# Optimization experiments

Measured on AMD Instinct MI355X. Metric: run time of the kernel, lower is better.

## Reference

```python
import jax, jax.numpy as jnp
import numpy as np

B, IN, OUT, T = 64, 1024, 512, 512
V_TH = 1.0
TAU = 16.0


def alpha_kernel(t, tau):
    # SRM alpha kernel: (t/tau)*exp(1 - t/tau) for t > 0, else 0.
    # Mask BEFORE exp to avoid overflow for large negative t.
    ts = jnp.where(t > 0, t, tau)
    v = (ts / tau) * jnp.exp(1.0 - ts / tau)
    return jnp.where(t > 0, v, 0.0)


def setup_inputs() -> dict:
    key = jax.random.key(0)
    k1, k2 = jax.random.split(key)
    # input spike times in [0, T/2)
    in_spike = jax.random.uniform(k1, (B, IN), dtype=jnp.float32) * (T / 2)
    weight = jax.random.normal(k2, (OUT, IN), dtype=jnp.float32) / np.float32(np.sqrt(IN))
    return {"in_spike": in_spike, "weight": weight}


def reference(in_spike, weight):
    t_seq = jnp.arange(T, dtype=jnp.float32)                  # [T]
    time_sequence = t_seq[None, None, :] - in_spike[:, :, None]  # [B, in, T]
    v_input = alpha_kernel(time_sequence, TAU)                 # [B, in, T]
    # fc applied along the `in` axis at every time step
    membrane_voltage = jnp.einsum('bit,oi->bot', v_input, weight)  # [B, out, T]
    # first time index where voltage crosses threshold; T if never.
    mask = membrane_voltage >= V_TH                            # [B, out, T]
    spiked = mask.any(axis=-1)
    first_t = jnp.argmax(mask, axis=-1)                        # first True index
    out_spike = jnp.where(spiked, first_t, T).astype(jnp.float32)  # [B, out]
    return out_spike
```

## Files before the change

kernel.cpp:

```cpp
#include <hip/hip_runtime.h>
#include <math.h>

#define BATCH   64
#define INS     1024
#define OUTS    512
#define TSTEPS  512
#define TAUF    16.0f

#define TT 64
#define NTRANS ((INS / TT) * (OUTS / TT))

__global__ __launch_bounds__(256) void pre_kernel(
        const float* __restrict__ w, float* __restrict__ wT,
        const float* __restrict__ in_spike, float4* __restrict__ spk) {
    __shared__ float tile[TT][TT + 1];
    __shared__ int hist[257];
    __shared__ int cursor[257];
    __shared__ int scanbuf[256];

    if (blockIdx.x < NTRANS) {
        const int i0 = (blockIdx.x & (INS / TT - 1)) * TT;
        const int o0 = (blockIdx.x / (INS / TT)) * TT;
        const int c  = threadIdx.x & 63;
        const int r  = threadIdx.x >> 6;
#pragma unroll
        for (int rr = r; rr < TT; rr += 4)
            tile[rr][c] = w[(o0 + rr) * INS + i0 + c];
        __syncthreads();
#pragma unroll
        for (int rr = r; rr < TT; rr += 4)
            wT[(i0 + rr) * OUTS + o0 + c] = tile[c][rr];
        return;
    }

    const int b = blockIdx.x - NTRANS;
    for (int k = threadIdx.x; k < 257; k += 256) hist[k] = 0;
    __syncthreads();

    float sv[INS / 256];
    int   tv[INS / 256];
#pragma unroll
    for (int j = 0; j < INS / 256; ++j) {
        int i = threadIdx.x + j * 256;
        float s = in_spike[b * INS + i];
        sv[j] = s;
        int t = (int)floorf(s) + 1;
        t = t < 1 ? 1 : (t > 256 ? 256 : t);
        tv[j] = t;
        atomicAdd(&hist[t], 1);
    }
    __syncthreads();

    const int tid = threadIdx.x;
    int v = hist[tid + 1];
    scanbuf[tid] = v;
    __syncthreads();
#pragma unroll
    for (int off = 1; off < 256; off <<= 1) {
        int add = (tid >= off) ? scanbuf[tid - off] : 0;
        __syncthreads();
        scanbuf[tid] += add;
        __syncthreads();
    }
    cursor[tid + 1] = scanbuf[tid] - v;
    __syncthreads();

#pragma unroll
    for (int j = 0; j < INS / 256; ++j) {
        int i = threadIdx.x + j * 256;
        int t = tv[j];
        int pos = atomicAdd(&cursor[t], 1);
        float A = expf(fmaf(sv[j], 1.0f / TAUF, 1.0f)) * (1.0f / TAUF);
        float C = -sv[j] * A;
        spk[b * INS + pos] =
            make_float4(A, __int_as_float(i * (OUTS / 2)), C, __int_as_float(t));
    }
}

#define OL 32
#define G  16
#define CH (INS / G)
#define TAIL0 257

__global__ __launch_bounds__(OL * G) void spike_scan_kernel(
        const float4* __restrict__ spk, const float* __restrict__ wT,
        float* __restrict__ out) {
    const int b = blockIdx.x;
    const int x = threadIdx.x;
    const int g = threadIdx.y;
    const int tid = g * OL + x;

    __shared__ float4 sspk[INS];
    __shared__ float  sE[TSTEPS];
    __shared__ float2 psA[G][OL];
    __shared__ float2 psC[G][OL];
    __shared__ int    sFirst[2 * OL];

    const float4* bspk = spk + b * INS;
    sspk[tid]           = bspk[tid];
    sspk[tid + OL * G]  = bspk[tid + OL * G];
    if (tid < TSTEPS) sE[tid] = expf((float)tid * (1.0f / TAUF));
    if (tid < 2 * OL) sFirst[tid] = TSTEPS;
    __syncthreads();

    const int k0 = g * CH;
    const float2* __restrict__ wT2 = (const float2*)wT;
    const int myo = blockIdx.y * OL + x;

    float pA0 = 0.f, pC0 = 0.f, pA1 = 0.f, pC1 = 0.f;
    for (int k = k0; k < k0 + CH; k += 4) {
        float4 p0 = sspk[k + 0];
        float4 p1 = sspk[k + 1];
        float4 p2 = sspk[k + 2];
        float4 p3 = sspk[k + 3];
        float2 w0 = wT2[__float_as_int(p0.y) + myo];
        float2 w1 = wT2[__float_as_int(p1.y) + myo];
        float2 w2 = wT2[__float_as_int(p2.y) + myo];
        float2 w3 = wT2[__float_as_int(p3.y) + myo];
        pA0 = fmaf(w0.x, p0.x, pA0); pC0 = fmaf(w0.x, p0.z, pC0);
        pA1 = fmaf(w0.y, p0.x, pA1); pC1 = fmaf(w0.y, p0.z, pC1);
        pA0 = fmaf(w1.x, p1.x, pA0); pC0 = fmaf(w1.x, p1.z, pC0);
        pA1 = fmaf(w1.y, p1.x, pA1); pC1 = fmaf(w1.y, p1.z, pC1);
        pA0 = fmaf(w2.x, p2.x, pA0); pC0 = fmaf(w2.x, p2.z, pC0);
        pA1 = fmaf(w2.y, p2.x, pA1); pC1 = fmaf(w2.y, p2.z, pC1);
        pA0 = fmaf(w3.x, p3.x, pA0); pC0 = fmaf(w3.x, p3.z, pC0);
        pA1 = fmaf(w3.y, p3.x, pA1); pC1 = fmaf(w3.y, p3.z, pC1);
    }
    psA[g][x] = make_float2(pA0, pA1);
    psC[g][x] = make_float2(pC0, pC1);
    __syncthreads();

    float SA0 = 0.f, SC0 = 0.f, SA1 = 0.f, SC1 = 0.f;
    float TA0 = 0.f, TC0 = 0.f, TA1 = 0.f, TC1 = 0.f;
    for (int j = 0; j < G; ++j) {
        float2 a = psA[j][x];
        float2 c = psC[j][x];
        if (j == g) { SA0 = TA0; SC0 = TC0; SA1 = TA1; SC1 = TC1; }
        TA0 += a.x; TC0 += c.x; TA1 += a.y; TC1 += c.y;
    }

    int tcur = __float_as_int(sspk[k0].w);
    const int tend = (g == G - 1) ? TAIL0 : __float_as_int(sspk[k0 + CH].w);

    int f0 = TSTEPS, f1 = TSTEPS;

#define ADVANCE_TO(TK)                                                        \
    while (tcur < (TK)) {                                                     \
        float e = sE[tcur]; float tf = (float)tcur;                           \
        if (f0 == TSTEPS && fmaf(tf, SA0, SC0) >= e) f0 = tcur;               \
        if (f1 == TSTEPS && fmaf(tf, SA1, SC1) >= e) f1 = tcur;               \
        if (f0 != TSTEPS && f1 != TSTEPS) goto pass2_done;                    \
        ++tcur;                                                               \
    }

    if (tcur >= tend || (sFirst[2 * x] <= tcur && sFirst[2 * x + 1] <= tcur))
        goto pass2_done;

    for (int k = k0; k < k0 + CH; k += 2) {
        float4 p0 = sspk[k + 0];
        float4 p1 = sspk[k + 1];
        float2 w0 = wT2[__float_as_int(p0.y) + myo];
        float2 w1 = wT2[__float_as_int(p1.y) + myo];
        int tk;
        tk = __float_as_int(p0.w); ADVANCE_TO(tk);
        SA0 = fmaf(w0.x, p0.x, SA0); SC0 = fmaf(w0.x, p0.z, SC0);
        SA1 = fmaf(w0.y, p0.x, SA1); SC1 = fmaf(w0.y, p0.z, SC1);
        tk = __float_as_int(p1.w); ADVANCE_TO(tk);
        SA0 = fmaf(w1.x, p1.x, SA0); SC0 = fmaf(w1.x, p1.z, SC0);
        SA1 = fmaf(w1.y, p1.x, SA1); SC1 = fmaf(w1.y, p1.z, SC1);
    }
    ADVANCE_TO(tend);
#undef ADVANCE_TO

pass2_done:
    {
        int ts = TAIL0 + (g << 4);
        if (ts < TSTEPS) {
            bool need0 = (f0 == TSTEPS) && (sFirst[2 * x]     > ts);
            bool need1 = (f1 == TSTEPS) && (sFirst[2 * x + 1] > ts);
            if (need0 | need1) {
                int te = ts + 16 > TSTEPS ? TSTEPS : ts + 16;
                for (int t = ts; t < te; ++t) {
                    float e = sE[t]; float tf = (float)t;
                    if (need0 && fmaf(tf, TA0, TC0) >= e) { f0 = t; need0 = false; }
                    if (need1 && fmaf(tf, TA1, TC1) >= e) { f1 = t; need1 = false; }
                }
            }
        }
    }

    if (f0 < TSTEPS) atomicMin(&sFirst[2 * x], f0);
    if (f1 < TSTEPS) atomicMin(&sFirst[2 * x + 1], f1);
    __syncthreads();
    if (tid < 2 * OL)
        out[b * OUTS + blockIdx.y * (2 * OL) + tid] = (float)sFirst[tid];
}

extern "C" void kernel_launch(void* const* d_in, const int* in_sizes, int n_in,
                              void* d_out, int out_size, void* d_ws, size_t ws_size,
                              hipStream_t stream) {
    const float* in_spike = (const float*)d_in[0];
    const float* weight   = (const float*)d_in[1];
    float* out = (float*)d_out;

    float*  wT  = (float*)d_ws;
    float4* spk = (float4*)((char*)d_ws + (size_t)INS * OUTS * sizeof(float));

    pre_kernel<<<NTRANS + BATCH, 256, 0, stream>>>(weight, wT, in_spike, spk);
    spike_scan_kernel<<<dim3(BATCH, OUTS / (2 * OL)), dim3(OL, G), 0, stream>>>(spk, wT, out);
}
```

Measured before the change: 95.67 us.

## Partition spike scan by time windows using per-batch bucket start offsets

The pre-kernel now writes per-batch bucket start offsets for spikes sorted by time. The scan kernel uses 32 groups, each owning a fixed 8-timestep window rather than an equal count of spikes, so each group knows its time range directly. Spikes are read straight from global memory instead of being staged in shared memory first, and the tail search past t=256 is split across groups in 8-step chunks. The risk is uneven load, because groups whose windows hold many spikes do more work, and the early-exit check against sFirst is removed.

```diff
diff --git a/kernel.cpp b/kernel.cpp
--- a/kernel.cpp
+++ b/kernel.cpp
@@ -12,7 +12,8 @@
 
 __global__ __launch_bounds__(256) void pre_kernel(
         const float* __restrict__ w, float* __restrict__ wT,
-        const float* __restrict__ in_spike, float4* __restrict__ spk) {
+        const float* __restrict__ in_spike, float4* __restrict__ spk,
+        int* __restrict__ starts) {
     __shared__ float tile[TT][TT + 1];
     __shared__ int hist[257];
     __shared__ int cursor[257];
@@ -62,7 +63,10 @@
         scanbuf[tid] += add;
         __syncthreads();
     }
-    cursor[tid + 1] = scanbuf[tid] - v;
+    int excl = scanbuf[tid] - v;
+    cursor[tid + 1] = excl;
+    starts[b * 258 + tid + 1] = excl;
+    if (tid == 0) { starts[b * 258] = 0; starts[b * 258 + 257] = INS; }
     __syncthreads();
 
 #pragma unroll
@@ -78,70 +82,52 @@
 }
 
 #define OL 32
-#define G  16
-#define CH (INS / G)
+#define G  32
+#define WS 8
 #define TAIL0 257
 
-__global__ __launch_bounds__(OL * G) void spike_scan_kernel(
-        const float4* __restrict__ spk, const float* __restrict__ wT,
-        float* __restrict__ out) {
+__global__ __launch_bounds__(OL * G, 8) void spike_scan_kernel(
+        const float4* __restrict__ spk, const int* __restrict__ starts,
+        const float* __restrict__ wT, float* __restrict__ out) {
     const int b = blockIdx.x;
     const int x = threadIdx.x;
     const int g = threadIdx.y;
     const int tid = g * OL + x;
 
-    __shared__ float4 sspk[INS];
+    __shared__ float4 ps[G][OL];
     __shared__ float  sE[TSTEPS];
-    __shared__ float2 psA[G][OL];
-    __shared__ float2 psC[G][OL];
     __shared__ int    sFirst[2 * OL];
 
-    const float4* bspk = spk + b * INS;
-    sspk[tid]           = bspk[tid];
-    sspk[tid + OL * G]  = bspk[tid + OL * G];
     if (tid < TSTEPS) sE[tid] = expf((float)tid * (1.0f / TAUF));
     if (tid < 2 * OL) sFirst[tid] = TSTEPS;
-    __syncthreads();
 
-    const int k0 = g * CH;
-    const float2* __restrict__ wT2 = (const float2*)wT;
-    const int myo = blockIdx.y * OL + x;
+    const float4* __restrict__ bspk = spk + b * INS;
+    const int* __restrict__ sb = starts + b * 258;
+    const int w0 = g * WS + 1;
+    const int kBeg = sb[w0];
+    const int kEnd = sb[w0 + WS];
+    const float2* __restrict__ wT2x = (const float2*)wT + (blockIdx.y * OL + x);
 
     float pA0 = 0.f, pC0 = 0.f, pA1 = 0.f, pC1 = 0.f;
-    for (int k = k0; k < k0 + CH; k += 4) {
-        float4 p0 = sspk[k + 0];
-        float4 p1 = sspk[k + 1];
-        float4 p2 = sspk[k + 2];
-        float4 p3 = sspk[k + 3];
-        float2 w0 = wT2[__float_as_int(p0.y) + myo];
-        float2 w1 = wT2[__float_as_int(p1.y) + myo];
-        float2 w2 = wT2[__float_as_int(p2.y) + myo];
-        float2 w3 = wT2[__float_as_int(p3.y) + myo];
-        pA0 = fmaf(w0.x, p0.x, pA0); pC0 = fmaf(w0.x, p0.z, pC0);
-        pA1 = fmaf(w0.y, p0.x, pA1); pC1 = fmaf(w0.y, p0.z, pC1);
-        pA0 = fmaf(w1.x, p1.x, pA0); pC0 = fmaf(w1.x, p1.z, pC0);
-        pA1 = fmaf(w1.y, p1.x, pA1); pC1 = fmaf(w1.y, p1.z, pC1);
-        pA0 = fmaf(w2.x, p2.x, pA0); pC0 = fmaf(w2.x, p2.z, pC0);
-        pA1 = fmaf(w2.y, p2.x, pA1); pC1 = fmaf(w2.y, p2.z, pC1);
-        pA0 = fmaf(w3.x, p3.x, pA0); pC0 = fmaf(w3.x, p3.z, pC0);
-        pA1 = fmaf(w3.y, p3.x, pA1); pC1 = fmaf(w3.y, p3.z, pC1);
+    for (int k = kBeg; k < kEnd; ++k) {
+        float4 p = bspk[k];
+        float2 w = wT2x[__float_as_int(p.y)];
+        pA0 = fmaf(w.x, p.x, pA0); pC0 = fmaf(w.x, p.z, pC0);
+        pA1 = fmaf(w.y, p.x, pA1); pC1 = fmaf(w.y, p.z, pC1);
     }
-    psA[g][x] = make_float2(pA0, pA1);
-    psC[g][x] = make_float2(pC0, pC1);
+    ps[g][x] = make_float4(pA0, pC0, pA1, pC1);
     __syncthreads();
 
     float SA0 = 0.f, SC0 = 0.f, SA1 = 0.f, SC1 = 0.f;
     float TA0 = 0.f, TC0 = 0.f, TA1 = 0.f, TC1 = 0.f;
     for (int j = 0; j < G; ++j) {
-        float2 a = psA[j][x];
-        float2 c = psC[j][x];
+        float4 q = ps[j][x];
         if (j == g) { SA0 = TA0; SC0 = TC0; SA1 = TA1; SC1 = TC1; }
-        TA0 += a.x; TC0 += c.x; TA1 += a.y; TC1 += c.y;
+        TA0 += q.x; TC0 += q.y; TA1 += q.z; TC1 += q.w;
     }
 
-    int tcur = __float_as_int(sspk[k0].w);
-    const int tend = (g == G - 1) ? TAIL0 : __float_as_int(sspk[k0 + CH].w);
-
+    int tcur = w0;
+    const int tend = w0 + WS;
     int f0 = TSTEPS, f1 = TSTEPS;
 
 #define ADVANCE_TO(TK)                                                        \
@@ -153,38 +139,28 @@
         ++tcur;                                                               \
     }
 
-    if (tcur >= tend || (sFirst[2 * x] <= tcur && sFirst[2 * x + 1] <= tcur))
-        goto pass2_done;
-
-    for (int k = k0; k < k0 + CH; k += 2) {
-        float4 p0 = sspk[k + 0];
-        float4 p1 = sspk[k + 1];
-        float2 w0 = wT2[__float_as_int(p0.y) + myo];
-        float2 w1 = wT2[__float_as_int(p1.y) + myo];
-        int tk;
-        tk = __float_as_int(p0.w); ADVANCE_TO(tk);
-        SA0 = fmaf(w0.x, p0.x, SA0); SC0 = fmaf(w0.x, p0.z, SC0);
-        SA1 = fmaf(w0.y, p0.x, SA1); SC1 = fmaf(w0.y, p0.z, SC1);
-        tk = __float_as_int(p1.w); ADVANCE_TO(tk);
-        SA0 = fmaf(w1.x, p1.x, SA0); SC0 = fmaf(w1.x, p1.z, SC0);
-        SA1 = fmaf(w1.y, p1.x, SA1); SC1 = fmaf(w1.y, p1.z, SC1);
+    for (int k = kBeg; k < kEnd; ++k) {
+        float4 p = bspk[k];
+        int tk = __float_as_int(p.w);
+        ADVANCE_TO(tk);
+        float2 w = wT2x[__float_as_int(p.y)];
+        SA0 = fmaf(w.x, p.x, SA0); SC0 = fmaf(w.x, p.z, SC0);
+        SA1 = fmaf(w.y, p.x, SA1); SC1 = fmaf(w.y, p.z, SC1);
     }
     ADVANCE_TO(tend);
 #undef ADVANCE_TO
 
 pass2_done:
     {
-        int ts = TAIL0 + (g << 4);
-        if (ts < TSTEPS) {
-            bool need0 = (f0 == TSTEPS) && (sFirst[2 * x]     > ts);
-            bool need1 = (f1 == TSTEPS) && (sFirst[2 * x + 1] > ts);
-            if (need0 | need1) {
-                int te = ts + 16 > TSTEPS ? TSTEPS : ts + 16;
-                for (int t = ts; t < te; ++t) {
-                    float e = sE[t]; float tf = (float)t;
-                    if (need0 && fmaf(tf, TA0, TC0) >= e) { f0 = t; need0 = false; }
-                    if (need1 && fmaf(tf, TA1, TC1) >= e) { f1 = t; need1 = false; }
-                }
+        int ts = TAIL0 + g * WS;
+        int te = ts + WS > TSTEPS ? TSTEPS : ts + WS;
+        bool need0 = (f0 == TSTEPS);
+        bool need1 = (f1 == TSTEPS);
+        if (need0 | need1) {
+            for (int t = ts; t < te; ++t) {
+                float e = sE[t]; float tf = (float)t;
+                if (need0 && fmaf(tf, TA0, TC0) >= e) { f0 = t; need0 = false; }
+                if (need1 && fmaf(tf, TA1, TC1) >= e) { f1 = t; need1 = false; }
             }
         }
     }
@@ -203,9 +179,12 @@
     const float* weight   = (const float*)d_in[1];
     float* out = (float*)d_out;
 
-    float*  wT  = (float*)d_ws;
-    float4* spk = (float4*)((char*)d_ws + (size_t)INS * OUTS * sizeof(float));
+    float*  wT     = (float*)d_ws;
+    float4* spk    = (float4*)((char*)d_ws + (size_t)INS * OUTS * sizeof(float));
+    int*    starts = (int*)((char*)d_ws + (size_t)INS * OUTS * sizeof(float)
+                                        + (size_t)BATCH * INS * sizeof(float4));
 
-    pre_kernel<<<NTRANS + BATCH, 256, 0, stream>>>(weight, wT, in_spike, spk);
-    spike_scan_kernel<<<dim3(BATCH, OUTS / (2 * OL)), dim3(OL, G), 0, stream>>>(spk, wT, out);
+    pre_kernel<<<NTRANS + BATCH, 256, 0, stream>>>(weight, wT, in_spike, spk, starts);
+    spike_scan_kernel<<<dim3(BATCH, OUTS / (2 * OL)), dim3(OL, G), 0, stream>>>(
+        spk, starts, wT, out);
 }
```

After: 110.5 us. 1.16x slower.
